# Kernel optimization log

Hardware: AMD Instinct MI355X
Metric: run time of the kernel (lower is better)

The kernel has to match this reference:

```python
import jax, jax.numpy as jnp
import numpy as np

K = 8  # number of nearest color neighbors
P = 2  # l2 mode


def setup_inputs() -> dict:
    key = jax.random.key(0)
    k1, k2 = jax.random.split(key)
    predictions = jax.random.uniform(k1, (4, 128, 8), dtype=jnp.float32)
    ref_imgs = jax.random.uniform(k2, (4, 3, 256, 256), dtype=jnp.float32)
    return {"predictions": predictions, "ref_imgs": ref_imgs}


def reference(predictions, ref_imgs):
    bs, L, _ = predictions.shape
    ch = ref_imgs.shape[1]
    img_size = ref_imgs.shape[-1]
    preds_position = predictions[:, :, :2]  # (bs, L, 2) normalized (x, y)

    # --- grid_sample(nearest, border, align_corners=False) color lookup ---
    # Original code flattens the grid bs-major ((i//L, i%L)) but tiles images
    # L-major (image index i % bs); we replicate that exact pairing.
    grid_flat = jax.lax.stop_gradient(preds_position).reshape(bs * L, 2)
    # unnormalize: x_pix = g * size - 0.5, then nearest + border clamp
    ix = jnp.clip(jnp.round(grid_flat[:, 0] * img_size - 0.5), 0, img_size - 1).astype(jnp.int32)
    iy = jnp.clip(jnp.round(grid_flat[:, 1] * img_size - 0.5), 0, img_size - 1).astype(jnp.int32)
    b_img = jnp.arange(bs * L, dtype=jnp.int32) % bs
    pooled_flat = ref_imgs[b_img, :, iy, ix]  # (bs*L, ch)
    # original rearrange '(L bs) ch 1 1 -> bs L ch 1 1': out[b,l] = flat[l*bs+b]
    pooled = pooled_flat.reshape(L, bs, ch).transpose(1, 0, 2)  # (bs, L, ch)

    # --- dense color-similarity map over the whole image ---
    sim = jnp.mean(jnp.abs(ref_imgs[:, None] - pooled[:, :, :, None, None]), axis=2)  # (bs, L, H, W)

    # --- topK best-matching pixel locations ---
    _, idx = jax.lax.top_k(-sim.reshape(bs, L, img_size * img_size), K)  # (bs, L, K)
    inv_size = jnp.float32(1.0 / img_size)
    tgt_y = (idx // img_size).astype(jnp.float32) * inv_size
    tgt_x = (idx % img_size).astype(jnp.float32) * inv_size
    tgt = jnp.stack([tgt_x, tgt_y], axis=-1)  # (bs, L, K, 2)
    tgt_down = jnp.roll(tgt, shift=1, axis=1)

    # --- min distance to previous stroke's candidate positions ---
    # cdist rows are identical (pred position repeated K times), so the
    # min over the last dim reduces to a single (bs, L, K) distance.
    diff = preds_position[:, :, None, :] - tgt_down  # (bs, L, K, 2)
    if P == 2:
        dist = jnp.sqrt(jnp.sum(diff * diff, axis=-1))
    else:
        dist = jnp.sum(jnp.abs(diff), axis=-1)
    val_down = jnp.min(dist, axis=-1)  # (bs, L)
    loss = jnp.mean(val_down[:, 1:])
    return loss
```

## Files before the change

kernel.cpp:

```cpp
#include <hip/hip_runtime.h>
#include <math.h>

#define BS 4
#define LQ 128
#define IMG 256
#define NPIX (IMG*IMG)
#define CAP 2048

__device__ __forceinline__ bool lessVI(float v1, int i1, float v2, int i2) {
    return (v1 < v2) || (v1 == v2 && i1 < i2);
}

__global__ __launch_bounds__(512)
void scan_kernel(const float* __restrict__ pred,
                 const float* __restrict__ imgs,
                 int* __restrict__ out_idx) {
    __shared__ float pool[2][3];
    __shared__ float ltau[2];
    __shared__ int   cnt[2];
    __shared__ float swv[8][8];
    __shared__ float lv[2][CAP];
    __shared__ int   li[2][CAP];

    const int bid = blockIdx.x;
    const int b  = (bid & 7) >> 1;
    const int qp = (bid >> 3) | ((bid & 1) << 5);
    const int tid  = threadIdx.x;
    const int qsel = tid >> 8;
    const int st   = tid & 255;
    const int l    = qp * 2 + qsel;

    const int n  = l * BS + b;
    const int pb = n >> 7;
    const int pl = n & (LQ - 1);
    const float px = pred[(pb * LQ + pl) * 8 + 0];
    const float py = pred[(pb * LQ + pl) * 8 + 1];
    const int ix = (int)fminf(fmaxf(rintf(px * 256.0f - 0.5f), 0.0f), 255.0f);
    const int iy = (int)fminf(fmaxf(rintf(py * 256.0f - 0.5f), 0.0f), 255.0f);
    const float* img = imgs + b * 3 * NPIX;
    const int pc = iy * IMG + ix;
    const float c0 = img[pc];
    const float c1 = img[NPIX + pc];
    const float c2 = img[2 * NPIX + pc];
    if (st == 0) {
        pool[qsel][0] = c0; pool[qsel][1] = c1; pool[qsel][2] = c2;
    }
    if (tid < 2) cnt[tid] = 0;

    float tb[8];
#pragma unroll
    for (int k = 0; k < 8; ++k) tb[k] = 3.0e38f;
    for (int j = 0; j < 16; ++j) {
        const int p = (st + j * 256) * 16;
        const float a0 = img[p];
        const float a1 = img[NPIX + p];
        const float a2 = img[2 * NPIX + p];
        const float s = fabsf(a0 - c0) + fabsf(a1 - c1) + fabsf(a2 - c2);
        if (s < tb[7]) {
            tb[7] = s;
#pragma unroll
            for (int k = 7; k > 0; --k) {
                if (tb[k] < tb[k - 1]) { float t = tb[k]; tb[k] = tb[k - 1]; tb[k - 1] = t; }
            }
        }
    }
#pragma unroll
    for (int off = 1; off < 64; off <<= 1) {
        float ov[8];
#pragma unroll
        for (int k = 0; k < 8; ++k) ov[k] = __shfl_xor(tb[k], off, 64);
        float w[8];
#pragma unroll
        for (int k = 0; k < 8; ++k) w[k] = fminf(tb[k], ov[7 - k]);
#define CEV(a, c) do { float lo = fminf(w[a], w[c]); float hi = fmaxf(w[a], w[c]); w[a] = lo; w[c] = hi; } while (0)
        CEV(0, 4); CEV(1, 5); CEV(2, 6); CEV(3, 7);
        CEV(0, 2); CEV(1, 3); CEV(4, 6); CEV(5, 7);
        CEV(0, 1); CEV(2, 3); CEV(4, 5); CEV(6, 7);
#undef CEV
#pragma unroll
        for (int k = 0; k < 8; ++k) tb[k] = w[k];
    }
    const int wid  = tid >> 6;
    const int lane = tid & 63;
    if (lane == 0) {
#pragma unroll
        for (int k = 0; k < 8; ++k) swv[wid][k] = tb[k];
    }
    __syncthreads();
    if ((tid & 255) == 0) {
        const int q = tid >> 8;
        const int base = q * 4;
        int ptr[4] = {0, 0, 0, 0};
        float last = 0.0f;
        for (int r = 0; r < 8; ++r) {
            int best = 0; float bvv = swv[base][ptr[0]];
            for (int w = 1; w < 4; ++w) {
                float vv = swv[base + w][ptr[w]];
                if (vv < bvv) { best = w; bvv = vv; }
            }
            last = bvv;
            ptr[best]++;
        }
        ltau[q] = last;
    }
    __syncthreads();

    const float t0 = ltau[0], t1 = ltau[1];
    const float q00 = pool[0][0], q01 = pool[0][1], q02 = pool[0][2];
    const float q10 = pool[1][0], q11 = pool[1][1], q12 = pool[1][2];
    const float4* i0 = (const float4*)img;
    const float4* i1 = (const float4*)(img + NPIX);
    const float4* i2 = (const float4*)(img + 2 * NPIX);

    for (int q4 = tid; q4 < NPIX / 4; q4 += 512) {
        const float4 a0 = i0[q4];
        const float4 a1 = i1[q4];
        const float4 a2 = i2[q4];
        const int p = q4 * 4;
#define PROC(vx, vy, vz, pix)                                                  \
        do {                                                                   \
            const float s0 = fabsf((vx) - q00) + fabsf((vy) - q01) + fabsf((vz) - q02); \
            if (s0 <= t0) {                                                    \
                const int pos = atomicAdd(&cnt[0], 1);                         \
                if (pos < CAP) { lv[0][pos] = s0; li[0][pos] = (pix); }        \
            }                                                                  \
            const float s1 = fabsf((vx) - q10) + fabsf((vy) - q11) + fabsf((vz) - q12); \
            if (s1 <= t1) {                                                    \
                const int pos = atomicAdd(&cnt[1], 1);                         \
                if (pos < CAP) { lv[1][pos] = s1; li[1][pos] = (pix); }        \
            }                                                                  \
        } while (0)
        PROC(a0.x, a1.x, a2.x, p + 0);
        PROC(a0.y, a1.y, a2.y, p + 1);
        PROC(a0.z, a1.z, a2.z, p + 2);
        PROC(a0.w, a1.w, a2.w, p + 3);
#undef PROC
    }
    __syncthreads();

    if ((wid & 3) == 0) {
        const int q = wid >> 2;
        const int nels = min(cnt[q], CAP);
        float bv[8]; int bi[8];
#pragma unroll
        for (int k = 0; k < 8; ++k) { bv[k] = 3.0e38f; bi[k] = 0x7FFFFFFF; }
        for (int c = lane; c < nels; c += 64) {
            const float v = lv[q][c];
            const int  id = li[q][c];
            if (lessVI(v, id, bv[7], bi[7])) {
                bv[7] = v; bi[7] = id;
#pragma unroll
                for (int k = 7; k > 0; --k) {
                    if (lessVI(bv[k], bi[k], bv[k - 1], bi[k - 1])) {
                        float tv = bv[k]; bv[k] = bv[k - 1]; bv[k - 1] = tv;
                        int   ti = bi[k]; bi[k] = bi[k - 1]; bi[k - 1] = ti;
                    }
                }
            }
        }
#pragma unroll
        for (int off = 1; off < 64; off <<= 1) {
            float ov[8]; int oi[8];
#pragma unroll
            for (int k = 0; k < 8; ++k) {
                ov[k] = __shfl_xor(bv[k], off, 64);
                oi[k] = __shfl_xor(bi[k], off, 64);
            }
            float w[8]; int wi[8];
#pragma unroll
            for (int k = 0; k < 8; ++k) {
                if (lessVI(bv[k], bi[k], ov[7 - k], oi[7 - k])) { w[k] = bv[k];     wi[k] = bi[k]; }
                else                                            { w[k] = ov[7 - k]; wi[k] = oi[7 - k]; }
            }
#define CE(a, c)                                                               \
            do {                                                               \
                if (lessVI(w[c], wi[c], w[a], wi[a])) {                        \
                    float tv = w[a]; w[a] = w[c]; w[c] = tv;                   \
                    int   ti = wi[a]; wi[a] = wi[c]; wi[c] = ti;               \
                }                                                              \
            } while (0)
            CE(0, 4); CE(1, 5); CE(2, 6); CE(3, 7);
            CE(0, 2); CE(1, 3); CE(4, 6); CE(5, 7);
            CE(0, 1); CE(2, 3); CE(4, 5); CE(6, 7);
#undef CE
#pragma unroll
            for (int k = 0; k < 8; ++k) { bv[k] = w[k]; bi[k] = wi[k]; }
        }
        if (lane == 0) {
            const int mq = b * LQ + qp * 2 + q;
            int* o = out_idx + mq * 8;
#pragma unroll
            for (int k = 0; k < 8; ++k) o[k] = bi[k];
        }
    }
}

__global__ __launch_bounds__(512)
void loss_kernel(const float* __restrict__ pred,
                 const int* __restrict__ idxs,
                 float* __restrict__ out) {
    __shared__ float red[512];
    const int t = threadIdx.x;
    const int b = t >> 7;
    const int l = t & (LQ - 1);
    float v = 0.0f;
    if (l >= 1) {
        const float px = pred[(b * LQ + l) * 8 + 0];
        const float py = pred[(b * LQ + l) * 8 + 1];
        const int* q = idxs + (b * LQ + (l - 1)) * 8;
        float best = 3.0e38f;
#pragma unroll
        for (int k = 0; k < 8; ++k) {
            const int id = q[k];
            const float tx = (float)(id & (IMG - 1)) * (1.0f / IMG);
            const float ty = (float)(id >> 8)        * (1.0f / IMG);
            const float dx = px - tx;
            const float dy = py - ty;
            best = fminf(best, sqrtf(dx * dx + dy * dy));
        }
        v = best;
    }
    red[t] = v;
    __syncthreads();
    for (int s = 256; s > 0; s >>= 1) {
        if (t < s) red[t] += red[t + s];
        __syncthreads();
    }
    if (t == 0) out[0] = red[0] * (1.0f / (BS * (LQ - 1)));
}

extern "C" void kernel_launch(void* const* d_in, const int* in_sizes, int n_in,
                              void* d_out, int out_size, void* d_ws, size_t ws_size,
                              hipStream_t stream) {
    const float* pred = (const float*)d_in[0];
    const float* imgs = (const float*)d_in[1];
    float* out = (float*)d_out;
    int* idx_ws = (int*)d_ws;

    hipLaunchKernelGGL(scan_kernel, dim3(256), dim3(512), 0, stream,
                       pred, imgs, idx_ws);
    hipLaunchKernelGGL(loss_kernel, dim3(1), dim3(512), 0, stream,
                       pred, idx_ws, out);
}
```

Before: 48.61 us.

## Split image scan into four slices per query pair and merge partial top-K

Each query pair's image scan is split across four blocks, each covering a quarter of the pixels. Each block builds a local threshold from a sample within its own slice and writes a partial top-8 of values and indices to the workspace. The loss kernel merges the four partial lists with a bitonic merge before computing distances. This quadruples the grid to use more CUs and shortens each block's serial scan, at the cost of more workspace traffic and merge work in the single-block loss kernel.

```diff
diff --git a/kernel.cpp b/kernel.cpp
--- a/kernel.cpp
+++ b/kernel.cpp
@@ -5,16 +5,41 @@
 #define LQ 128
 #define IMG 256
 #define NPIX (IMG*IMG)
-#define CAP 2048
+#define NSLICE 4
+#define SLICE_PIX (NPIX/NSLICE)
+#define SLICE_F4  (SLICE_PIX/4)
+#define CAP 512
 
 __device__ __forceinline__ bool lessVI(float v1, int i1, float v2, int i2) {
     return (v1 < v2) || (v1 == v2 && i1 < i2);
 }
+
+#define CE8(WV, WI, a, c)                                                     \
+    do {                                                                      \
+        if (lessVI((WV)[c], (WI)[c], (WV)[a], (WI)[a])) {                     \
+            float tv_ = (WV)[a]; (WV)[a] = (WV)[c]; (WV)[c] = tv_;            \
+            int   ti_ = (WI)[a]; (WI)[a] = (WI)[c]; (WI)[c] = ti_;            \
+        }                                                                     \
+    } while (0)
+
+#define MERGE8(AV, AI, BV, BI, OV, OI)                                        \
+    do {                                                                      \
+        _Pragma("unroll")                                                     \
+        for (int k_ = 0; k_ < 8; ++k_) {                                      \
+            if (lessVI((AV)[k_], (AI)[k_], (BV)[7-k_], (BI)[7-k_])) {         \
+                (OV)[k_] = (AV)[k_]; (OI)[k_] = (AI)[k_];                     \
+            } else { (OV)[k_] = (BV)[7-k_]; (OI)[k_] = (BI)[7-k_]; }          \
+        }                                                                     \
+        CE8(OV, OI, 0, 4); CE8(OV, OI, 1, 5); CE8(OV, OI, 2, 6); CE8(OV, OI, 3, 7); \
+        CE8(OV, OI, 0, 2); CE8(OV, OI, 1, 3); CE8(OV, OI, 4, 6); CE8(OV, OI, 5, 7); \
+        CE8(OV, OI, 0, 1); CE8(OV, OI, 2, 3); CE8(OV, OI, 4, 5); CE8(OV, OI, 6, 7); \
+    } while (0)
 
 __global__ __launch_bounds__(512)
 void scan_kernel(const float* __restrict__ pred,
                  const float* __restrict__ imgs,
-                 int* __restrict__ out_idx) {
+                 float* __restrict__ wsv,
+                 int* __restrict__ wsi) {
     __shared__ float pool[2][3];
     __shared__ float ltau[2];
     __shared__ int   cnt[2];
@@ -24,7 +49,9 @@
 
     const int bid = blockIdx.x;
     const int b  = (bid & 7) >> 1;
-    const int qp = (bid >> 3) | ((bid & 1) << 5);
+    const int u  = bid >> 3;
+    const int sl = u & (NSLICE - 1);
+    const int qp = (u >> 2) | ((bid & 1) << 5);
     const int tid  = threadIdx.x;
     const int qsel = tid >> 8;
     const int st   = tid & 255;
@@ -50,8 +77,9 @@
     float tb[8];
 #pragma unroll
     for (int k = 0; k < 8; ++k) tb[k] = 3.0e38f;
+#pragma unroll 4
     for (int j = 0; j < 16; ++j) {
-        const int p = (st + j * 256) * 16;
+        const int p = sl * SLICE_PIX + j * 1024 + st;
         const float a0 = img[p];
         const float a1 = img[NPIX + p];
         const float a2 = img[2 * NPIX + p];
@@ -112,7 +140,10 @@
     const float4* i1 = (const float4*)(img + NPIX);
     const float4* i2 = (const float4*)(img + 2 * NPIX);
 
-    for (int q4 = tid; q4 < NPIX / 4; q4 += 512) {
+    const int base4 = sl * SLICE_F4;
+#pragma unroll 2
+    for (int it = 0; it < SLICE_F4 / 512; ++it) {
+        const int q4 = base4 + it * 512 + tid;
         const float4 a0 = i0[q4];
         const float4 a1 = i1[q4];
         const float4 a2 = i2[q4];
@@ -172,32 +203,25 @@
                 if (lessVI(bv[k], bi[k], ov[7 - k], oi[7 - k])) { w[k] = bv[k];     wi[k] = bi[k]; }
                 else                                            { w[k] = ov[7 - k]; wi[k] = oi[7 - k]; }
             }
-#define CE(a, c)                                                               \
-            do {                                                               \
-                if (lessVI(w[c], wi[c], w[a], wi[a])) {                        \
-                    float tv = w[a]; w[a] = w[c]; w[c] = tv;                   \
-                    int   ti = wi[a]; wi[a] = wi[c]; wi[c] = ti;               \
-                }                                                              \
-            } while (0)
-            CE(0, 4); CE(1, 5); CE(2, 6); CE(3, 7);
-            CE(0, 2); CE(1, 3); CE(4, 6); CE(5, 7);
-            CE(0, 1); CE(2, 3); CE(4, 5); CE(6, 7);
-#undef CE
+            CE8(w, wi, 0, 4); CE8(w, wi, 1, 5); CE8(w, wi, 2, 6); CE8(w, wi, 3, 7);
+            CE8(w, wi, 0, 2); CE8(w, wi, 1, 3); CE8(w, wi, 4, 6); CE8(w, wi, 5, 7);
+            CE8(w, wi, 0, 1); CE8(w, wi, 2, 3); CE8(w, wi, 4, 5); CE8(w, wi, 6, 7);
 #pragma unroll
             for (int k = 0; k < 8; ++k) { bv[k] = w[k]; bi[k] = wi[k]; }
         }
         if (lane == 0) {
             const int mq = b * LQ + qp * 2 + q;
-            int* o = out_idx + mq * 8;
-#pragma unroll
-            for (int k = 0; k < 8; ++k) o[k] = bi[k];
+            const int slot = mq * (NSLICE * 8) + sl * 8;
+#pragma unroll
+            for (int k = 0; k < 8; ++k) { wsv[slot + k] = bv[k]; wsi[slot + k] = bi[k]; }
         }
     }
 }
 
 __global__ __launch_bounds__(512)
 void loss_kernel(const float* __restrict__ pred,
-                 const int* __restrict__ idxs,
+                 const float* __restrict__ wsv,
+                 const int* __restrict__ wsi,
                  float* __restrict__ out) {
     __shared__ float red[512];
     const int t = threadIdx.x;
@@ -205,13 +229,29 @@
     const int l = t & (LQ - 1);
     float v = 0.0f;
     if (l >= 1) {
+        const int mq = b * LQ + (l - 1);
+        float av[4][8]; int ai[4][8];
+#pragma unroll
+        for (int s = 0; s < 4; ++s) {
+#pragma unroll
+            for (int k = 0; k < 8; ++k) {
+                av[s][k] = wsv[mq * 32 + s * 8 + k];
+                ai[s][k] = wsi[mq * 32 + s * 8 + k];
+            }
+        }
+        float m0v[8]; int m0i[8];
+        float m1v[8]; int m1i[8];
+        float fv[8];  int fi[8];
+        MERGE8(av[0], ai[0], av[1], ai[1], m0v, m0i);
+        MERGE8(av[2], ai[2], av[3], ai[3], m1v, m1i);
+        MERGE8(m0v, m0i, m1v, m1i, fv, fi);
+
         const float px = pred[(b * LQ + l) * 8 + 0];
         const float py = pred[(b * LQ + l) * 8 + 1];
-        const int* q = idxs + (b * LQ + (l - 1)) * 8;
         float best = 3.0e38f;
 #pragma unroll
         for (int k = 0; k < 8; ++k) {
-            const int id = q[k];
+            const int id = fi[k];
             const float tx = (float)(id & (IMG - 1)) * (1.0f / IMG);
             const float ty = (float)(id >> 8)        * (1.0f / IMG);
             const float dx = px - tx;
@@ -235,10 +275,11 @@
     const float* pred = (const float*)d_in[0];
     const float* imgs = (const float*)d_in[1];
     float* out = (float*)d_out;
-    int* idx_ws = (int*)d_ws;
-
-    hipLaunchKernelGGL(scan_kernel, dim3(256), dim3(512), 0, stream,
-                       pred, imgs, idx_ws);
+    float* wsv = (float*)d_ws;
+    int*   wsi = (int*)((char*)d_ws + 512 * 32 * sizeof(float));
+
+    hipLaunchKernelGGL(scan_kernel, dim3(BS * 64 * NSLICE), dim3(512), 0, stream,
+                       pred, imgs, wsv, wsi);
     hipLaunchKernelGGL(loss_kernel, dim3(1), dim3(512), 0, stream,
-                       pred, idx_ws, out);
-}
+                       pred, wsv, wsi, out);
+}
```

Result: faster. 41.76 us (-14.1%).
